# Kernel optimization log

Measured on AMD Instinct MI355X. Metric: run time of the kernel, lower is better.

Reference implementation:

```python
import jax, jax.numpy as jnp
import numpy as np

# ---- module config (init_kwargs) ----
LAT = 512          # lat_size
OUT_SIZE = 32768   # out_size
NF = 128           # n_filter
NCALLS = 4         # n_calls
CUBE = int(np.ceil(OUT_SIZE ** (1.0 / 3.0)))  # 32
CF = 3             # SinSobel c_factor for dim=3 (one sin-sobel gradient per axis)
FIN, FH, FO = NF * CF, NF, NF
# hypernet output: w_in(FH,FIN)+b_in(FH)+w_mid(FH,FH)+b_mid(FH)+w_out(FO,FH)+b_out(FO)+w_short(FO,FIN)+b_short(FO)
KTOT = FH * FIN + FH + FH * FH + FH + FO * FH + FO + FO * FIN + FO  # 131584
EPS = 1e-5


def _inorm(x):
    # InstanceNorm3d, affine=False: normalize each (b, c) over D,H,W
    m = x.mean(axis=(2, 3, 4), keepdims=True)
    v = x.var(axis=(2, 3, 4), keepdims=True)
    return (x - m) * jax.lax.rsqrt(v + EPS)


def _sobel_kernel():
    # SinSobel: fixed sinusoidal sobel gradient along each of the 3 axes
    g = jnp.sin(jnp.linspace(-1.0, 1.0, 3) * (jnp.pi / 2.0))  # [-1, 0, 1]
    kx = jnp.broadcast_to(g[:, None, None], (3, 3, 3))
    ky = jnp.broadcast_to(g[None, :, None], (3, 3, 3))
    kz = jnp.broadcast_to(g[None, None, :], (3, 3, 3))
    base = jnp.stack([kx, ky, kz])[:, None]          # (3, 1, 3, 3, 3)
    return jnp.tile(base, (NF, 1, 1, 1, 1))           # (NF*3, 1, 3, 3, 3) depthwise


def setup_inputs() -> dict:
    key = jax.random.key(0)
    k1, k2, k3, k4 = jax.random.split(key, 4)
    B = 4
    lat = jax.random.normal(k1, (B, LAT), jnp.float32)
    seed = jax.random.normal(k2, (1, NF, CUBE, CUBE, CUBE), jnp.float32)
    W_k = jax.random.normal(k3, (LAT, KTOT), jnp.float32) * 0.02  # hypernet weight
    b_k = jax.random.normal(k4, (KTOT,), jnp.float32) * 0.02      # hypernet bias
    return {"lat": lat, "seed": seed, "W_k": W_k, "b_k": b_k}


def _forward(lat, seed, W_k, b_k):
    B = lat.shape[0]
    V = CUBE ** 3
    # hypernetwork: per-sample dynamic 1x1x1 conv weights
    ks = lat @ W_k + b_k  # (B, KTOT)
    idx = [0]
    def take(n, shape):
        w = ks[:, idx[0]:idx[0] + n].reshape((B,) + shape)
        idx[0] += n
        return w
    w_in = take(FH * FIN, (FH, FIN)); b_in = take(FH, (FH, 1))
    w_mid = take(FH * FH, (FH, FH));  b_mid = take(FH, (FH, 1))
    w_out = take(FO * FH, (FO, FH));  b_out = take(FO, (FO, 1))
    w_sh = take(FO * FIN, (FO, FIN)); b_sh = take(FO, (FO, 1))

    sob = _sobel_kernel()
    out = _inorm(jnp.tile(seed, (B, 1, 1, 1, 1)))  # seed_norm

    def body(out, _):
        # fixed depthwise sin-sobel conv3d: (B,NF,S,S,S) -> (B,3*NF,S,S,S)
        y = jax.lax.conv_general_dilated(
            out, sob, (1, 1, 1), 'SAME',
            dimension_numbers=('NCDHW', 'OIDHW', 'NCDHW'),
            feature_group_count=NF)
        y = _inorm(y).reshape(B, FIN, V)
        # DynaResidualBlock: per-sample 1x1x1 convs == batched matmuls
        h = jax.nn.relu(jnp.einsum('bcv,bhc->bhv', y, w_in) + b_in)
        h = jax.nn.relu(jnp.einsum('bcv,bhc->bhv', h, w_mid) + b_mid)
        h = jnp.einsum('bcv,boc->bov', h, w_out) + b_out
        s = jnp.einsum('bcv,boc->bov', y, w_sh) + b_sh
        y = (h + s).reshape(B, NF, CUBE, CUBE, CUBE)
        return out + 0.1 * y, None

    out, _ = jax.lax.scan(body, out, None, length=NCALLS)
    return out.mean(1).reshape(B, -1)[:, :OUT_SIZE]


def reference(lat, seed, W_k, b_k):
    return _forward(lat, seed, W_k, b_k)
```

## Files before the change

kernel.cpp:

```cpp
#include <hip/hip_runtime.h>
#include <cstdint>
#include <cstddef>

#define BB 4
#define LATN 512
#define NFC 128
#define FIN 384
#define KTOT 131584
#define VV 32768
#define NCALLS 4

typedef unsigned short u16;
typedef unsigned int u32;
typedef __bf16 v8bf __attribute__((ext_vector_type(8)));
typedef float v4f __attribute__((ext_vector_type(4)));

__device__ inline u16 f2bf(float f) {
  u32 u = __builtin_bit_cast(u32, f);
  u += 0x7fffu + ((u >> 16) & 1u);
  return (u16)(u >> 16);
}

__global__ __launch_bounds__(256) void k_hyper(const float* __restrict__ lat,
    const float* __restrict__ Wk, const float* __restrict__ bk,
    float* __restrict__ ks, u16* __restrict__ wbf)
{
  __shared__ float lats[BB * LATN];
  int tid = threadIdx.x;
  for (int i = tid; i < BB * LATN; i += 256) lats[i] = lat[i];
  __syncthreads();
  int k = blockIdx.x * 256 + tid;
  float a0 = 0.f, a1 = 0.f, a2 = 0.f, a3 = 0.f;
  for (int l = 0; l < LATN; ++l) {
    float w = Wk[(size_t)l * KTOT + k];
    a0 = fmaf(w, lats[l], a0);
    a1 = fmaf(w, lats[LATN + l], a1);
    a2 = fmaf(w, lats[2 * LATN + l], a2);
    a3 = fmaf(w, lats[3 * LATN + l], a3);
  }
  float bv = bk[k];
  a0 += bv; a1 += bv; a2 += bv; a3 += bv;
  ks[k] = a0; ks[KTOT + k] = a1; ks[2 * (size_t)KTOT + k] = a2; ks[3 * (size_t)KTOT + k] = a3;
  wbf[k] = f2bf(a0); wbf[KTOT + k] = f2bf(a1);
  wbf[2 * (size_t)KTOT + k] = f2bf(a2); wbf[3 * (size_t)KTOT + k] = f2bf(a3);
}

__global__ __launch_bounds__(256) void k_seednorm(const float* __restrict__ seed,
                                                  float* __restrict__ outb)
{
  int c = blockIdx.x;
  const float* s = seed + (size_t)c * VV;
  int tid = threadIdx.x;
  float sum = 0.f, sq = 0.f;
  for (int v = tid; v < VV; v += 256) { float x = s[v]; sum += x; sq = fmaf(x, x, sq); }
  #pragma unroll
  for (int off = 32; off; off >>= 1) { sum += __shfl_down(sum, off); sq += __shfl_down(sq, off); }
  __shared__ float r0[4], r1[4]; __shared__ float mb, rb;
  int wid = tid >> 6, lid = tid & 63;
  if (lid == 0) { r0[wid] = sum; r1[wid] = sq; }
  __syncthreads();
  if (tid == 0) {
    float st = r0[0] + r0[1] + r0[2] + r0[3];
    float qt = r1[0] + r1[1] + r1[2] + r1[3];
    float m = st / (float)VV;
    float var = qt / (float)VV - m * m;
    mb = m; rb = rsqrtf(var + 1e-5f);
  }
  __syncthreads();
  float m = mb, r = rb;
  for (int v = tid; v < VV; v += 256) {
    float x = (s[v] - m) * r;
    outb[(size_t)(0 * NFC + c) * VV + v] = x;
    outb[(size_t)(1 * NFC + c) * VV + v] = x;
    outb[(size_t)(2 * NFC + c) * VV + v] = x;
    outb[(size_t)(3 * NFC + c) * VV + v] = x;
  }
}

__global__ __launch_bounds__(256) void k_conv(const float* __restrict__ outb,
    u16* __restrict__ yb, float* __restrict__ stats)
{
  int bc = blockIdx.x;
  const float* x = outb + (size_t)bc * VV;
  int b = bc >> 7, c = bc & 127;
  u16* y0 = yb + (size_t)(b * FIN + 3 * c) * VV;
  float s0 = 0, q0 = 0, s1 = 0, q1 = 0, s2 = 0, q2 = 0;
  for (int rr = threadIdx.x; rr < 1024; rr += 256) {
    int d = rr >> 5, h = rr & 31;
    float g1[32], g2[32], g3[32];
    #pragma unroll
    for (int i = 0; i < 32; ++i) { g1[i] = 0.f; g2[i] = 0.f; g3[i] = 0.f; }
    for (int dd = -1; dd <= 1; ++dd) {
      int D = d + dd; if ((unsigned)D >= 32u) continue;
      float fd = (float)dd;
      for (int dh = -1; dh <= 1; ++dh) {
        int H = h + dh; if ((unsigned)H >= 32u) continue;
        float fh = (float)dh;
        const float4* rp = (const float4*)(x + (D << 10) + (H << 5));
        #pragma unroll
        for (int w4 = 0; w4 < 8; ++w4) {
          float4 v = rp[w4];
          int base = w4 * 4;
          g1[base + 0] = fmaf(fd, v.x, g1[base + 0]); g2[base + 0] = fmaf(fh, v.x, g2[base + 0]); g3[base + 0] += v.x;
          g1[base + 1] = fmaf(fd, v.y, g1[base + 1]); g2[base + 1] = fmaf(fh, v.y, g2[base + 1]); g3[base + 1] += v.y;
          g1[base + 2] = fmaf(fd, v.z, g1[base + 2]); g2[base + 2] = fmaf(fh, v.z, g2[base + 2]); g3[base + 2] += v.z;
          g1[base + 3] = fmaf(fd, v.w, g1[base + 3]); g2[base + 3] = fmaf(fh, v.w, g2[base + 3]); g3[base + 3] += v.w;
        }
      }
    }
    int rowoff = rr << 5;
    u16 pa[32], pe[32], pz[32];
    #pragma unroll
    for (int w = 0; w < 32; ++w) {
      float a = g1[w] + (w > 0 ? g1[w - 1] : 0.f) + (w < 31 ? g1[w + 1] : 0.f);
      float e = g2[w] + (w > 0 ? g2[w - 1] : 0.f) + (w < 31 ? g2[w + 1] : 0.f);
      float z = (w < 31 ? g3[w + 1] : 0.f) - (w > 0 ? g3[w - 1] : 0.f);
      s0 += a; q0 = fmaf(a, a, q0);
      s1 += e; q1 = fmaf(e, e, q1);
      s2 += z; q2 = fmaf(z, z, q2);
      pa[w] = f2bf(a); pe[w] = f2bf(e); pz[w] = f2bf(z);
    }
    #pragma unroll
    for (int w8 = 0; w8 < 4; ++w8) {
      *(uint4*)(y0 + rowoff + w8 * 8) = *(uint4*)(pa + w8 * 8);
      *(uint4*)(y0 + (size_t)VV + rowoff + w8 * 8) = *(uint4*)(pe + w8 * 8);
      *(uint4*)(y0 + 2 * (size_t)VV + rowoff + w8 * 8) = *(uint4*)(pz + w8 * 8);
    }
  }
  float vals[6] = { s0, q0, s1, q1, s2, q2 };
  __shared__ float red[6][4];
  int wid = threadIdx.x >> 6, lid = threadIdx.x & 63;
  #pragma unroll
  for (int t = 0; t < 6; ++t) {
    float v = vals[t];
    #pragma unroll
    for (int off = 32; off; off >>= 1) v += __shfl_down(v, off);
    if (lid == 0) red[t][wid] = v;
  }
  __syncthreads();
  if (threadIdx.x == 0) {
    #pragma unroll
    for (int a = 0; a < 3; ++a) {
      float st = red[2 * a][0] + red[2 * a][1] + red[2 * a][2] + red[2 * a][3];
      float qt = red[2 * a + 1][0] + red[2 * a + 1][1] + red[2 * a + 1][2] + red[2 * a + 1][3];
      float m = st / (float)VV;
      float var = qt / (float)VV - m * m;
      float rs = rsqrtf(var + 1e-5f);
      int oc = b * FIN + 3 * c + a;
      stats[2 * oc] = m; stats[2 * oc + 1] = rs;
    }
  }
}

__global__ __launch_bounds__(128) void k_prep(const float* __restrict__ ks,
    const float* __restrict__ stats, u16* __restrict__ wbf, float* __restrict__ badj)
{
  int b = blockIdx.x >> 1, which = blockIdx.x & 1;
  int h = threadIdx.x;
  const float* ksb = ks + (size_t)b * KTOT;
  const float2* st = (const float2*)(stats + b * FIN * 2);
  int woff = which ? 82304 : 0;
  const float* ws = ksb + woff + h * FIN;
  u16* wd = wbf + (size_t)b * KTOT + woff + h * FIN;
  float accm = 0.f;
  for (int cc = 0; cc < FIN; ++cc) {
    float2 mr = st[cc];
    float sw = ws[cc] * mr.y;
    wd[cc] = f2bf(sw);
    accm = fmaf(sw, mr.x, accm);
  }
  int boff = which ? 131456 : 49152;
  badj[b * 256 + which * 128 + h] = ksb[boff + h] - accm;
}

#define WPAD 34
#define WBUF (32 * WPAD)
#define WREG (2 * WBUF)

__device__ inline void phaseR(const u16* __restrict__ A, const u16* __restrict__ X,
                              int K, int ln, int quad, int n0, v4f acc[8][2])
{
  const u16* x0 = X + (size_t)(n0 + ln) * K + quad * 8;
  const u16* x1 = X + (size_t)(n0 + 16 + ln) * K + quad * 8;
  const u16* ap = A + (size_t)ln * K + quad * 8;
  #pragma unroll 2
  for (int k0 = 0; k0 < K; k0 += 32) {
    v8bf bf0 = *(const v8bf*)(x0 + k0);
    v8bf bf1 = *(const v8bf*)(x1 + k0);
    #pragma unroll
    for (int mt = 0; mt < 8; ++mt) {
      v8bf av = *(const v8bf*)(ap + (size_t)mt * 16 * K + k0);
      acc[mt][0] = __builtin_amdgcn_mfma_f32_16x16x32_bf16(av, bf0, acc[mt][0], 0, 0, 0);
      acc[mt][1] = __builtin_amdgcn_mfma_f32_16x16x32_bf16(av, bf1, acc[mt][1], 0, 0, 0);
    }
  }
}

__device__ inline void phaseT(const u16* __restrict__ Ab, const u16* __restrict__ Xb,
                              int K, int n0blk, int tid, u16* xs, v4f acc[8][2])
{
  int lane = tid & 63, wave = tid >> 6;
  int ln = lane & 15, quad = lane >> 4;
  int nw = n0blk + wave * 32;
  u16* wb = xs + wave * WREG;
  int nch = K >> 5;
  int kr0 = lane >> 2;
  int ch  = lane & 3;
  const u16* src = Xb + (size_t)kr0 * VV + nw + ch * 8;
  const u16* ap0 = Ab + (size_t)ln * K + quad * 8;

  uint4 ra = *(const uint4*)(src);
  uint4 rb = *(const uint4*)(src + (size_t)16 * VV);

  for (int c = 0; c < nch; ++c) {
    u16* bufc = wb + (c & 1) * WBUF;
    *(uint4*)(bufc + kr0 * WPAD + ch * 8) = ra;
    *(uint4*)(bufc + (kr0 + 16) * WPAD + ch * 8) = rb;
    v8bf av[8];
    const u16* ap = ap0 + (c << 5);
    #pragma unroll
    for (int mt = 0; mt < 8; ++mt) av[mt] = *(const v8bf*)(ap + (size_t)mt * 16 * K);
    if (c + 1 < nch) {
      const u16* s2 = src + (size_t)(c + 1) * 32 * VV;
      ra = *(const uint4*)(s2);
      rb = *(const uint4*)(s2 + (size_t)16 * VV);
    }
    #pragma unroll
    for (int nt = 0; nt < 2; ++nt) {
      union { u16 u[8]; v8bf v; } bu;
      #pragma unroll
      for (int j = 0; j < 8; ++j) bu.u[j] = bufc[(quad * 8 + j) * WPAD + nt * 16 + ln];
      #pragma unroll
      for (int mt = 0; mt < 8; ++mt)
        acc[mt][nt] = __builtin_amdgcn_mfma_f32_16x16x32_bf16(av[mt], bu.v, acc[mt][nt], 0, 0, 0);
    }
  }
}

template <int MODE>
__global__ __launch_bounds__(256) void k_gemm(
    const u16* __restrict__ A1, const u16* __restrict__ X1, int K1,
    const u16* __restrict__ A2, const u16* __restrict__ X2, int K2,
    const float* __restrict__ bias1, int bstr1,
    const float* __restrict__ bias2, int bstr2,
    u16* __restrict__ outH, float* __restrict__ outAcc, int relu)
{
  extern __shared__ u16 xs[];
  int b = blockIdx.y;
  int tid = threadIdx.x;
  int lane = tid & 63, wave = tid >> 6;
  int ln = lane & 15, quad = lane >> 4;
  int n0blk = blockIdx.x * 128;
  v4f acc[8][2];
  #pragma unroll
  for (int i = 0; i < 8; ++i)
    for (int j = 0; j < 2; ++j) acc[i][j] = (v4f){0.f, 0.f, 0.f, 0.f};

  if (MODE == 0) {
    phaseT(A1 + (size_t)b * KTOT, X1 + (size_t)b * K1 * VV, K1, n0blk, tid, xs, acc);
  } else if (MODE == 1) {
    phaseR(A1 + (size_t)b * KTOT, X1 + (size_t)b * K1 * VV, K1, ln, quad,
           n0blk + wave * 32, acc);
  } else {
    phaseR(A1 + (size_t)b * KTOT, X1 + (size_t)b * K1 * VV, K1, ln, quad,
           n0blk + wave * 32, acc);
    phaseT(A2 + (size_t)b * KTOT, X2 + (size_t)b * K2 * VV, K2, n0blk, tid, xs, acc);
  }

  const float* b1 = bias1 + (size_t)b * bstr1;
  const float* b2 = bias2 ? bias2 + (size_t)b * bstr2 : nullptr;
  #pragma unroll
  for (int nt = 0; nt < 2; ++nt) {
    int n = n0blk + wave * 32 + nt * 16 + ln;
    #pragma unroll
    for (int mt = 0; mt < 8; ++mt) {
      float v[4];
      #pragma unroll
      for (int r = 0; r < 4; ++r) {
        int m = mt * 16 + quad * 4 + r;
        float t = acc[mt][nt][r] + b1[m];
        if (b2) t += b2[m];
        if (relu) t = fmaxf(t, 0.f);
        v[r] = t;
      }
      if (outH) {
        ushort4 pk = make_ushort4(f2bf(v[0]), f2bf(v[1]), f2bf(v[2]), f2bf(v[3]));
        *(ushort4*)(outH + ((size_t)b * VV + n) * 128 + mt * 16 + quad * 4) = pk;
      } else {
        #pragma unroll
        for (int r = 0; r < 4; ++r) {
          int m = mt * 16 + quad * 4 + r;
          outAcc[(size_t)(b * 128 + m) * VV + n] += 0.1f * v[r];
        }
      }
    }
  }
}

__global__ __launch_bounds__(256) void k_mean(const float* __restrict__ outb,
                                              float* __restrict__ dout)
{
  int idx = blockIdx.x * 256 + threadIdx.x;
  int b = idx >> 15, v = idx & (VV - 1);
  const float* p = outb + (size_t)b * NFC * VV + v;
  float s = 0.f;
  for (int c = 0; c < NFC; ++c) s += p[(size_t)c * VV];
  dout[idx] = s * (1.0f / (float)NFC);
}

extern "C" void kernel_launch(void* const* d_in, const int* in_sizes, int n_in,
                              void* d_out, int out_size, void* d_ws, size_t ws_size,
                              hipStream_t stream)
{
  const float* lat  = (const float*)d_in[0];
  const float* seed = (const float*)d_in[1];
  const float* Wk   = (const float*)d_in[2];
  const float* bk   = (const float*)d_in[3];

  char* p = (char*)d_ws;
  float* ks    = (float*)p; p += (size_t)BB * KTOT * 4;
  u16*   wbf   = (u16*)p;   p += (size_t)BB * KTOT * 2;
  float* badj  = (float*)p; p += (size_t)BB * 256 * 4;
  float* stats = (float*)p; p += (size_t)BB * FIN * 2 * 4;
  float* outb  = (float*)p; p += (size_t)BB * NFC * VV * 4;
  u16*   yb    = (u16*)p;   p += (size_t)BB * FIN * VV * 2;
  u16*   h1    = (u16*)p;   p += (size_t)BB * 128 * VV * 2;
  u16*   h2    = (u16*)p;   p += (size_t)BB * 128 * VV * 2;
  (void)ws_size; (void)in_sizes; (void)n_in; (void)out_size;

  const size_t TLDS = (size_t)4 * WREG * sizeof(u16);

  k_hyper<<<dim3(KTOT / 256), 256, 0, stream>>>(lat, Wk, bk, ks, wbf);
  k_seednorm<<<dim3(NFC), 256, 0, stream>>>(seed, outb);

  for (int t = 0; t < NCALLS; ++t) {
    k_conv<<<dim3(BB * NFC), 256, 0, stream>>>(outb, yb, stats);
    k_prep<<<dim3(8), 128, 0, stream>>>(ks, stats, wbf, badj);
    k_gemm<0><<<dim3(VV / 128, BB), 256, TLDS, stream>>>(
        wbf + 0, yb, FIN, nullptr, nullptr, 0,
        badj + 0, 256, nullptr, 0, h1, nullptr, 1);
    k_gemm<1><<<dim3(VV / 128, BB), 256, 0, stream>>>(
        wbf + 49280, h1, 128, nullptr, nullptr, 0,
        ks + 65664, KTOT, nullptr, 0, h2, nullptr, 1);
    k_gemm<2><<<dim3(VV / 128, BB), 256, TLDS, stream>>>(
        wbf + 65792, h2, 128, wbf + 82304, yb, FIN,
        ks + 82176, KTOT, badj + 128, 256, nullptr, outb, 0);
  }
  k_mean<<<dim3((BB * VV) / 256), 256, 0, stream>>>(outb, (float*)d_out);
}
```

Measured before the change: 1.826 ms.

## Transpose conv output to voxel-major layout once, drop LDS transpose path in GEMMs

Adds a k_trans kernel that converts the channel-major bf16 conv output into a voxel-major copy. The first and last GEMMs can then use the register-only phaseR path instead of the LDS-staged phaseT transpose. This removes the per-GEMM LDS shuffle and the redundant transposed reads of y in two GEMMs. In exchange it costs an extra kernel launch, one more full read and write of y per iteration, and a larger workspace.

```diff
diff --git a/kernel.cpp b/kernel.cpp
--- a/kernel.cpp
+++ b/kernel.cpp
@@ -152,6 +152,36 @@
   }
 }
 
+__global__ __launch_bounds__(256) void k_trans(const u16* __restrict__ yb,
+                                               u16* __restrict__ yt)
+{
+  int b = blockIdx.x >> 7;
+  int vtile = blockIdx.x & 127;
+  int tid = threadIdx.x;
+  int wave = tid >> 6, lane = tid & 63;
+  int vi = lane >> 3, ki = lane & 7;
+  int v0 = vtile * 256 + wave * 64 + vi * 8;
+  const u16* src = yb + (size_t)b * FIN * VV;
+  u16* dst = yt + (size_t)b * VV * FIN;
+  union U { uint4 q; u16 s[8]; };
+  #pragma unroll
+  for (int kb = 0; kb < 6; ++kb) {
+    int k0 = kb * 64 + ki * 8;
+    U r[8], c[8];
+    #pragma unroll
+    for (int i = 0; i < 8; ++i)
+      r[i].q = *(const uint4*)(src + (size_t)(k0 + i) * VV + v0);
+    #pragma unroll
+    for (int j = 0; j < 8; ++j) {
+      #pragma unroll
+      for (int i = 0; i < 8; ++i) c[j].s[i] = r[i].s[j];
+    }
+    #pragma unroll
+    for (int j = 0; j < 8; ++j)
+      *(uint4*)(dst + (size_t)(v0 + j) * FIN + k0) = c[j].q;
+  }
+}
+
 __global__ __launch_bounds__(128) void k_prep(const float* __restrict__ ks,
     const float* __restrict__ stats, u16* __restrict__ wbf, float* __restrict__ badj)
 {
@@ -173,10 +203,6 @@
   badj[b * 256 + which * 128 + h] = ksb[boff + h] - accm;
 }
 
-#define WPAD 34
-#define WBUF (32 * WPAD)
-#define WREG (2 * WBUF)
-
 __device__ inline void phaseR(const u16* __restrict__ A, const u16* __restrict__ X,
                               int K, int ln, int quad, int n0, v4f acc[8][2])
 {
@@ -196,48 +222,7 @@
   }
 }
 
-__device__ inline void phaseT(const u16* __restrict__ Ab, const u16* __restrict__ Xb,
-                              int K, int n0blk, int tid, u16* xs, v4f acc[8][2])
-{
-  int lane = tid & 63, wave = tid >> 6;
-  int ln = lane & 15, quad = lane >> 4;
-  int nw = n0blk + wave * 32;
-  u16* wb = xs + wave * WREG;
-  int nch = K >> 5;
-  int kr0 = lane >> 2;
-  int ch  = lane & 3;
-  const u16* src = Xb + (size_t)kr0 * VV + nw + ch * 8;
-  const u16* ap0 = Ab + (size_t)ln * K + quad * 8;
-
-  uint4 ra = *(const uint4*)(src);
-  uint4 rb = *(const uint4*)(src + (size_t)16 * VV);
-
-  for (int c = 0; c < nch; ++c) {
-    u16* bufc = wb + (c & 1) * WBUF;
-    *(uint4*)(bufc + kr0 * WPAD + ch * 8) = ra;
-    *(uint4*)(bufc + (kr0 + 16) * WPAD + ch * 8) = rb;
-    v8bf av[8];
-    const u16* ap = ap0 + (c << 5);
-    #pragma unroll
-    for (int mt = 0; mt < 8; ++mt) av[mt] = *(const v8bf*)(ap + (size_t)mt * 16 * K);
-    if (c + 1 < nch) {
-      const u16* s2 = src + (size_t)(c + 1) * 32 * VV;
-      ra = *(const uint4*)(s2);
-      rb = *(const uint4*)(s2 + (size_t)16 * VV);
-    }
-    #pragma unroll
-    for (int nt = 0; nt < 2; ++nt) {
-      union { u16 u[8]; v8bf v; } bu;
-      #pragma unroll
-      for (int j = 0; j < 8; ++j) bu.u[j] = bufc[(quad * 8 + j) * WPAD + nt * 16 + ln];
-      #pragma unroll
-      for (int mt = 0; mt < 8; ++mt)
-        acc[mt][nt] = __builtin_amdgcn_mfma_f32_16x16x32_bf16(av[mt], bu.v, acc[mt][nt], 0, 0, 0);
-    }
-  }
-}
-
-template <int MODE>
+template <int TWO>
 __global__ __launch_bounds__(256) void k_gemm(
     const u16* __restrict__ A1, const u16* __restrict__ X1, int K1,
     const u16* __restrict__ A2, const u16* __restrict__ X2, int K2,
@@ -245,33 +230,25 @@
     const float* __restrict__ bias2, int bstr2,
     u16* __restrict__ outH, float* __restrict__ outAcc, int relu)
 {
-  extern __shared__ u16 xs[];
   int b = blockIdx.y;
   int tid = threadIdx.x;
   int lane = tid & 63, wave = tid >> 6;
   int ln = lane & 15, quad = lane >> 4;
-  int n0blk = blockIdx.x * 128;
+  int n0 = blockIdx.x * 128 + wave * 32;
   v4f acc[8][2];
   #pragma unroll
   for (int i = 0; i < 8; ++i)
     for (int j = 0; j < 2; ++j) acc[i][j] = (v4f){0.f, 0.f, 0.f, 0.f};
 
-  if (MODE == 0) {
-    phaseT(A1 + (size_t)b * KTOT, X1 + (size_t)b * K1 * VV, K1, n0blk, tid, xs, acc);
-  } else if (MODE == 1) {
-    phaseR(A1 + (size_t)b * KTOT, X1 + (size_t)b * K1 * VV, K1, ln, quad,
-           n0blk + wave * 32, acc);
-  } else {
-    phaseR(A1 + (size_t)b * KTOT, X1 + (size_t)b * K1 * VV, K1, ln, quad,
-           n0blk + wave * 32, acc);
-    phaseT(A2 + (size_t)b * KTOT, X2 + (size_t)b * K2 * VV, K2, n0blk, tid, xs, acc);
-  }
+  phaseR(A1 + (size_t)b * KTOT, X1 + (size_t)b * K1 * VV, K1, ln, quad, n0, acc);
+  if (TWO)
+    phaseR(A2 + (size_t)b * KTOT, X2 + (size_t)b * K2 * VV, K2, ln, quad, n0, acc);
 
   const float* b1 = bias1 + (size_t)b * bstr1;
   const float* b2 = bias2 ? bias2 + (size_t)b * bstr2 : nullptr;
   #pragma unroll
   for (int nt = 0; nt < 2; ++nt) {
-    int n = n0blk + wave * 32 + nt * 16 + ln;
+    int n = n0 + nt * 16 + ln;
     #pragma unroll
     for (int mt = 0; mt < 8; ++mt) {
       float v[4];
@@ -324,26 +301,26 @@
   float* stats = (float*)p; p += (size_t)BB * FIN * 2 * 4;
   float* outb  = (float*)p; p += (size_t)BB * NFC * VV * 4;
   u16*   yb    = (u16*)p;   p += (size_t)BB * FIN * VV * 2;
+  u16*   yt    = (u16*)p;   p += (size_t)BB * VV * FIN * 2;
   u16*   h1    = (u16*)p;   p += (size_t)BB * 128 * VV * 2;
   u16*   h2    = (u16*)p;   p += (size_t)BB * 128 * VV * 2;
   (void)ws_size; (void)in_sizes; (void)n_in; (void)out_size;
 
-  const size_t TLDS = (size_t)4 * WREG * sizeof(u16);
-
   k_hyper<<<dim3(KTOT / 256), 256, 0, stream>>>(lat, Wk, bk, ks, wbf);
   k_seednorm<<<dim3(NFC), 256, 0, stream>>>(seed, outb);
 
   for (int t = 0; t < NCALLS; ++t) {
     k_conv<<<dim3(BB * NFC), 256, 0, stream>>>(outb, yb, stats);
+    k_trans<<<dim3(512), 256, 0, stream>>>(yb, yt);
     k_prep<<<dim3(8), 128, 0, stream>>>(ks, stats, wbf, badj);
-    k_gemm<0><<<dim3(VV / 128, BB), 256, TLDS, stream>>>(
-        wbf + 0, yb, FIN, nullptr, nullptr, 0,
+    k_gemm<0><<<dim3(VV / 128, BB), 256, 0, stream>>>(
+        wbf + 0, yt, FIN, nullptr, nullptr, 0,
         badj + 0, 256, nullptr, 0, h1, nullptr, 1);
-    k_gemm<1><<<dim3(VV / 128, BB), 256, 0, stream>>>(
+    k_gemm<0><<<dim3(VV / 128, BB), 256, 0, stream>>>(
         wbf + 49280, h1, 128, nullptr, nullptr, 0,
         ks + 65664, KTOT, nullptr, 0, h2, nullptr, 1);
-    k_gemm<2><<<dim3(VV / 128, BB), 256, TLDS, stream>>>(
-        wbf + 65792, h2, 128, wbf + 82304, yb, FIN,
+    k_gemm<1><<<dim3(VV / 128, BB), 256, 0, stream>>>(
+        wbf + 65792, h2, 128, wbf + 82304, yt, FIN,
         ks + 82176, KTOT, badj + 128, 256, nullptr, outb, 0);
   }
   k_mean<<<dim3((BB * VV) / 256), 256, 0, stream>>>(outb, (float*)d_out);
```

After: 2.126 ms. 16.4% more time.
